# Kernel optimization log

Hardware: AMD Instinct MI355X
Metric: run time of the kernel (lower is better)

## Reference

```python
import math
import jax, jax.numpy as jnp
import numpy as np

B, N, M = 8, 2048, 1024
INPUT_SIZE = 512
HEAD_DIM = 64
NUM_HEADS = 6
ATTN_SIZE = HEAD_DIM * NUM_HEADS
MAX_CLASSES = 512


def setup_inputs() -> dict:
    key = jax.random.key(0)
    k1, k2, k3, k4, k5, k6, k7 = jax.random.split(key, 7)
    bound = 1.0 / math.sqrt(INPUT_SIZE)
    return {
        "train_embeddings": jax.random.normal(k1, (B, N, INPUT_SIZE), jnp.float32),
        "test_embeddings": jax.random.normal(k2, (B, M, INPUT_SIZE), jnp.float32),
        "targets": jax.random.randint(k3, (B, N), 0, MAX_CLASSES),
        # torch nn.Linear weights, stored as [in, out] for direct matmul
        "Wq": jax.random.uniform(k4, (INPUT_SIZE, ATTN_SIZE), jnp.float32, -bound, bound),
        "bq": jax.random.uniform(k5, (ATTN_SIZE,), jnp.float32, -bound, bound),
        "Wk": jax.random.uniform(k6, (INPUT_SIZE, ATTN_SIZE), jnp.float32, -bound, bound),
        "bk": jax.random.uniform(k7, (ATTN_SIZE,), jnp.float32, -bound, bound),
    }


def reference(train_embeddings, test_embeddings, targets, Wq, bq, Wk, bk):
    b, m, _ = test_embeddings.shape
    # projections -> [B, S, H, D]
    q_bmhd = (test_embeddings @ Wq + bq).reshape(b, m, NUM_HEADS, HEAD_DIM)
    k_bnhd = (train_embeddings @ Wk + bk).reshape(b, -1, NUM_HEADS, HEAD_DIM)
    scale = 1.0 / math.sqrt(HEAD_DIM)  # SDPA default scale
    # attention scores [B, H, M, N]
    scores = jnp.einsum("bmhd,bnhd->bhmn", q_bmhd, k_bnhd) * scale
    attn = jax.nn.softmax(scores, axis=-1)
    # one-hot train targets [B, N, C]; chunk-folding in the torch code is a
    # memory trick — mathematically it is just attn @ one_hot per head
    onehot_bnc = jax.nn.one_hot(targets, MAX_CLASSES, dtype=q_bmhd.dtype)
    out_bhmc = jnp.einsum("bhmn,bnc->bhmc", attn, onehot_bnc)
    out_bmc = out_bhmc.mean(axis=1)          # mean over heads
    out_mbc = out_bmc.transpose(1, 0, 2)      # [M, B, C]
    return jnp.log(jnp.clip(out_mbc, 1e-05) + 3e-05)
```

## Files before the change

kernel.cpp:

```cpp
#include <hip/hip_runtime.h>
#include <hip/hip_bf16.h>

#define BQ 8
#define NN 2048
#define MM 1024
#define EE 512
#define NH 6
#define AA 384
#define CC 512

#define KROW_B (AA * 2)
#define TILE_B (16 * KROW_B)
#define WROW_B (EE * 2)
#define WTILE_B (16 * WROW_B)

#define QSCALE 0.1803368801111204f

typedef __bf16 bf16x8 __attribute__((ext_vector_type(8)));
typedef float  f32x4  __attribute__((ext_vector_type(4)));
using bf16 = __hip_bfloat16;

static __device__ __forceinline__ f32x4 mfma16(bf16x8 a, bf16x8 b, f32x4 c) {
  return __builtin_amdgcn_mfma_f32_16x16x32_bf16(a, b, c, 0, 0, 0);
}

typedef __attribute__((address_space(1))) const void gconst_void;
typedef __attribute__((address_space(3))) void lds_void_t;
static __device__ __forceinline__ void ld_lds16(const void* g, void* l) {
  __builtin_amdgcn_global_load_lds((gconst_void*)g, (lds_void_t*)l, 16, 0, 0);
}

static __device__ __forceinline__ unsigned short f2bfu(float x) {
  union { __hip_bfloat16 h; unsigned short u; } v;
  v.h = __float2bfloat16(x);
  return v.u;
}
static __device__ __forceinline__ float bf2f(unsigned short u) {
  union { unsigned int i; float f; } x;
  x.i = ((unsigned int)u) << 16;
  return x.f;
}

__global__ __launch_bounds__(256) void transw_kernel(const float* __restrict__ W, bf16* __restrict__ WT) {
  __shared__ float t[64][65];
  int kb = (blockIdx.x / 6) * 64, nb = (blockIdx.x % 6) * 64;
  int tid = threadIdx.x;
  int lr = tid >> 4, lc = (tid & 15) * 4;
  #pragma unroll
  for (int p = 0; p < 4; p++) {
    int k = lr + p * 16;
    float4 v = *reinterpret_cast<const float4*>(W + (size_t)(kb + k) * AA + nb + lc);
    t[k][lc] = v.x; t[k][lc + 1] = v.y; t[k][lc + 2] = v.z; t[k][lc + 3] = v.w;
  }
  __syncthreads();
  #pragma unroll
  for (int p = 0; p < 4; p++) {
    int n = lr + p * 16;
    bf16* dst = WT + (size_t)(nb + n) * EE + kb + lc;
    dst[0] = __float2bfloat16(t[lc][n]);
    dst[1] = __float2bfloat16(t[lc + 1][n]);
    dst[2] = __float2bfloat16(t[lc + 2][n]);
    dst[3] = __float2bfloat16(t[lc + 3][n]);
  }
}

__global__ __launch_bounds__(512) void build_kernel(const int* __restrict__ targets,
                                                    int* __restrict__ offs, int* __restrict__ idxs) {
  __shared__ int cnt[CC], ssum[CC], pos[CC];
  int b = blockIdx.x, tid = threadIdx.x;
  cnt[tid] = 0;
  __syncthreads();
  int t[4];
  #pragma unroll
  for (int i = 0; i < 4; i++) {
    t[i] = targets[b * NN + tid * 4 + i];
    atomicAdd(&cnt[t[i]], 1);
  }
  __syncthreads();
  ssum[tid] = cnt[tid];
  __syncthreads();
  for (int d = 1; d < CC; d <<= 1) {
    int v = (tid >= d) ? ssum[tid - d] : 0;
    __syncthreads();
    ssum[tid] += v;
    __syncthreads();
  }
  int excl = ssum[tid] - cnt[tid];
  offs[b * (CC + 1) + tid] = excl;
  if (tid == CC - 1) offs[b * (CC + 1) + CC] = NN;
  pos[tid] = excl;
  __syncthreads();
  #pragma unroll
  for (int i = 0; i < 4; i++) {
    int p = atomicAdd(&pos[t[i]], 1);
    idxs[b * NN + p] = tid * 4 + i;
  }
}

__global__ __launch_bounds__(256, 3) void proj_kernel(
    const float* __restrict__ test, const float* __restrict__ train,
    const bf16* __restrict__ WqT, const bf16* __restrict__ WkT,
    const float* __restrict__ bq, const float* __restrict__ bk,
    bf16* __restrict__ Qb, bf16* __restrict__ Kb)
{
  __shared__ char wbuf[3][WTILE_B];
  int tid = threadIdx.x, wid = tid >> 6, lane = tid & 63;
  int bid = blockIdx.x;
  int sub = bid & 1, unit = bid >> 1;
  const float* A; const bf16* WT; const float* bias; bf16* C; float scale; int m0;
  if (unit < 128) { A = test;  WT = WqT; bias = bq; C = Qb; scale = QSCALE; m0 = unit * 64; }
  else            { A = train; WT = WkT; bias = bk; C = Kb; scale = 1.0f;   m0 = (unit - 128) * 64; }
  m0 += wid * 16;
  int row = lane & 15, hi = lane >> 4;

  bf16x8 af[16];
  const float* arow = A + (size_t)(m0 + row) * EE + hi * 8;
  #pragma unroll
  for (int ks = 0; ks < 16; ks++) {
    float4 u = *reinterpret_cast<const float4*>(arow + ks * 32);
    float4 v = *reinterpret_cast<const float4*>(arow + ks * 32 + 4);
    bf16x8 f;
    f[0] = (__bf16)u.x; f[1] = (__bf16)u.y; f[2] = (__bf16)u.z; f[3] = (__bf16)u.w;
    f[4] = (__bf16)v.x; f[5] = (__bf16)v.y; f[6] = (__bf16)v.z; f[7] = (__bf16)v.w;
    af[ks] = f;
  }

  int ldso[4], srco[4];
  #pragma unroll
  for (int i = 0; i < 4; i++) {
    int off = tid * 16 + i * 4096;
    int rw = off >> 10, c = off & 1023;
    ldso[i] = off;
    srco[i] = rw * WROW_B + (c ^ ((rw & 7) << 4));
  }
  const char* wgbase = (const char*)WT + (size_t)sub * 12 * WTILE_B;
  int sw = (row & 7) << 4;

  auto stage = [&](int t, int buf) {
    const char* src = wgbase + (size_t)t * WTILE_B;
    #pragma unroll
    for (int i = 0; i < 4; i++) ld_lds16(src + srco[i], wbuf[buf] + ldso[i]);
  };
  auto compute = [&](int buf, int t) {
    const char* wb = wbuf[buf] + row * WROW_B;
    f32x4 acc0 = {0.f, 0.f, 0.f, 0.f}, acc1 = {0.f, 0.f, 0.f, 0.f};
    #pragma unroll
    for (int ks = 0; ks < 16; ks += 2) {
      bf16x8 w0 = *reinterpret_cast<const bf16x8*>(wb + ((hi * 16 + ks * 64) ^ sw));
      bf16x8 w1 = *reinterpret_cast<const bf16x8*>(wb + ((hi * 16 + (ks + 1) * 64) ^ sw));
      acc0 = mfma16(af[ks], w0, acc0);
      acc1 = mfma16(af[ks + 1], w1, acc1);
    }
    f32x4 acc = acc0 + acc1;
    int ocol = (sub * 12 + t) * 16 + row;
    float bv = bias[ocol];
    #pragma unroll
    for (int j = 0; j < 4; j++)
      C[(size_t)(m0 + hi * 4 + j) * AA + ocol] = __float2bfloat16((acc[j] + bv) * scale);
  };

  stage(0, 0);
  stage(1, 1);
  asm volatile("s_waitcnt vmcnt(4)" ::: "memory");
  __builtin_amdgcn_s_barrier();
  __builtin_amdgcn_sched_barrier(0);
  stage(2, 2);
  compute(0, 0);

  int cur = 1, stg = 0;
  #pragma unroll 1
  for (int t = 1; t < 11; t++) {
    asm volatile("s_waitcnt vmcnt(8)" ::: "memory");
    __builtin_amdgcn_s_barrier();
    __builtin_amdgcn_sched_barrier(0);
    if (t < 10) stage(t + 2, stg);
    compute(cur, t);
    cur = cur + 1 < 3 ? cur + 1 : 0;
    stg = stg + 1 < 3 ? stg + 1 : 0;
  }
  asm volatile("s_waitcnt vmcnt(4)" ::: "memory");
  __builtin_amdgcn_s_barrier();
  __builtin_amdgcn_sched_barrier(0);
  compute(cur, 11);
}

__global__ __launch_bounds__(256, 4) void zpass_kernel(
    const bf16* __restrict__ Qb, const bf16* __restrict__ Kb, float* __restrict__ Zp)
{
  __shared__ char kbuf[3][TILE_B];
  int id = blockIdx.x;
  int b = id & 7, r = id >> 3, mt = r & 15, nc = r >> 4;
  int tid = threadIdx.x, wid = tid >> 6, lane = tid & 63;
  int m0 = mt * 64 + wid * 16, n0 = nc * 256;
  int row = lane & 15, hi = lane >> 4;

  bf16x8 qf[12];
  const bf16* qrow = Qb + ((size_t)(b * MM + m0 + row)) * AA + hi * 8;
  #pragma unroll
  for (int ks = 0; ks < 12; ks++) qf[ks] = *reinterpret_cast<const bf16x8*>(qrow + ks * 32);

  int ldso[3], srco[3];
  #pragma unroll
  for (int i = 0; i < 3; i++) {
    int off = wid * 3072 + i * 1024 + lane * 16;
    int rw = off / KROW_B, c = off - rw * KROW_B;
    ldso[i] = off;
    srco[i] = rw * KROW_B + (c ^ ((rw & 7) << 4));
  }
  const char* kgbase = (const char*)(Kb + ((size_t)(b * NN + n0)) * AA);

  int sw = (row & 7) << 4;
  int rbase = row * KROW_B;
  int x0 = rbase + ((hi * 16) ^ sw);
  int x1 = rbase + (((hi * 16) + 64) ^ sw);

  float zacc[NH][4];
  #pragma unroll
  for (int h = 0; h < NH; h++)
    #pragma unroll
    for (int j = 0; j < 4; j++) zacc[h][j] = 0.f;

  auto stage = [&](int t, int buf) {
    const char* src = kgbase + (size_t)t * TILE_B;
    #pragma unroll
    for (int i = 0; i < 3; i++) ld_lds16(src + srco[i], kbuf[buf] + ldso[i]);
  };
  auto compute = [&](int buf) {
    const char* kb = kbuf[buf];
    #pragma unroll
    for (int h = 0; h < NH; h++) {
      bf16x8 k0 = *reinterpret_cast<const bf16x8*>(kb + h * 128 + x0);
      bf16x8 k1 = *reinterpret_cast<const bf16x8*>(kb + h * 128 + x1);
      f32x4 acc = {0.f, 0.f, 0.f, 0.f};
      acc = mfma16(qf[2 * h], k0, acc);
      acc = mfma16(qf[2 * h + 1], k1, acc);
      #pragma unroll
      for (int j = 0; j < 4; j++) zacc[h][j] += __builtin_amdgcn_exp2f(acc[j]);
    }
  };

  stage(0, 0);
  stage(1, 1);
  int cur = 0, stg = 2;
  #pragma unroll 1
  for (int nt = 0; nt < 15; nt++) {
    asm volatile("s_waitcnt vmcnt(3)" ::: "memory");
    __builtin_amdgcn_s_barrier();
    __builtin_amdgcn_sched_barrier(0);
    if (nt < 14) stage(nt + 2, stg);
    compute(cur);
    cur = cur + 1 < 3 ? cur + 1 : 0;
    stg = stg + 1 < 3 ? stg + 1 : 0;
  }
  asm volatile("s_waitcnt vmcnt(0)" ::: "memory");
  __builtin_amdgcn_s_barrier();
  __builtin_amdgcn_sched_barrier(0);
  compute(cur);

  #pragma unroll
  for (int h = 0; h < NH; h++)
    #pragma unroll
    for (int j = 0; j < 4; j++) {
      float v = zacc[h][j];
      v += __shfl_xor(v, 1); v += __shfl_xor(v, 2);
      v += __shfl_xor(v, 4); v += __shfl_xor(v, 8);
      zacc[h][j] = v;
    }
  if (row == 0) {
    #pragma unroll
    for (int h = 0; h < NH; h++)
      #pragma unroll
      for (int j = 0; j < 4; j++)
        Zp[(((size_t)nc * 8 + b) * NH + h) * MM + m0 + hi * 4 + j] = zacc[h][j];
  }
}

__global__ __launch_bounds__(256, 4) void wpass_kernel(
    const bf16* __restrict__ Qb, const bf16* __restrict__ Kb,
    const float* __restrict__ Zp, bf16* __restrict__ W2)
{
  __shared__ char kbuf[3][TILE_B];
  int id = blockIdx.x;
  int b = id & 7, r = id >> 3, mt = r & 15, nc = r >> 4;
  int tid = threadIdx.x, wid = tid >> 6, lane = tid & 63;
  int m0 = mt * 64 + wid * 16, n0 = nc * 256;
  int row = lane & 15, hi = lane >> 4;

  bf16x8 qf[12];
  const bf16* qrow = Qb + ((size_t)(b * MM + m0 + row)) * AA + hi * 8;
  #pragma unroll
  for (int ks = 0; ks < 12; ks++) qf[ks] = *reinterpret_cast<const bf16x8*>(qrow + ks * 32);

  float rz[NH][4];
  #pragma unroll
  for (int h = 0; h < NH; h++) {
    f32x4 z = {0.f, 0.f, 0.f, 0.f};
    #pragma unroll
    for (int p = 0; p < 8; p++)
      z += *reinterpret_cast<const f32x4*>(Zp + (((size_t)p * 8 + b) * NH + h) * MM + m0 + hi * 4);
    #pragma unroll
    for (int j = 0; j < 4; j++) rz[h][j] = 1.0f / (6.0f * z[j]);
  }

  int ldso[3], srco[3];
  #pragma unroll
  for (int i = 0; i < 3; i++) {
    int off = wid * 3072 + i * 1024 + lane * 16;
    int rw = off / KROW_B, c = off - rw * KROW_B;
    ldso[i] = off;
    srco[i] = rw * KROW_B + (c ^ ((rw & 7) << 4));
  }
  const char* kgbase = (const char*)(Kb + ((size_t)(b * NN + n0)) * AA);

  int sw = (row & 7) << 4;
  int rbase = row * KROW_B;
  int x0 = rbase + ((hi * 16) ^ sw);
  int x1 = rbase + (((hi * 16) + 64) ^ sw);

  int m4 = (m0 >> 2) + hi;

  auto stage = [&](int t, int buf) {
    const char* src = kgbase + (size_t)t * TILE_B;
    #pragma unroll
    for (int i = 0; i < 3; i++) ld_lds16(src + srco[i], kbuf[buf] + ldso[i]);
  };
  auto compute = [&](int buf, int nt) {
    const char* kb = kbuf[buf];
    float w0 = 0.f, w1 = 0.f, w2 = 0.f, w3 = 0.f;
    #pragma unroll
    for (int h = 0; h < NH; h++) {
      bf16x8 k0 = *reinterpret_cast<const bf16x8*>(kb + h * 128 + x0);
      bf16x8 k1 = *reinterpret_cast<const bf16x8*>(kb + h * 128 + x1);
      f32x4 acc = {0.f, 0.f, 0.f, 0.f};
      acc = mfma16(qf[2 * h], k0, acc);
      acc = mfma16(qf[2 * h + 1], k1, acc);
      w0 += __builtin_amdgcn_exp2f(acc[0]) * rz[h][0];
      w1 += __builtin_amdgcn_exp2f(acc[1]) * rz[h][1];
      w2 += __builtin_amdgcn_exp2f(acc[2]) * rz[h][2];
      w3 += __builtin_amdgcn_exp2f(acc[3]) * rz[h][3];
    }
    int n = n0 + nt * 16 + row;
    ushort4 q;
    q.x = f2bfu(w0); q.y = f2bfu(w1); q.z = f2bfu(w2); q.w = f2bfu(w3);
    *reinterpret_cast<ushort4*>((unsigned short*)W2 + (((size_t)(b * 256 + m4)) * NN + n) * 4) = q;
  };

  stage(0, 0);
  stage(1, 1);
  asm volatile("s_waitcnt vmcnt(3)" ::: "memory");
  __builtin_amdgcn_s_barrier();
  __builtin_amdgcn_sched_barrier(0);
  stage(2, 2);
  compute(0, 0);

  int cur = 1, stg = 0;
  #pragma unroll 1
  for (int nt = 1; nt < 15; nt++) {
    asm volatile("s_waitcnt vmcnt(7)" ::: "memory");
    __builtin_amdgcn_s_barrier();
    __builtin_amdgcn_sched_barrier(0);
    if (nt < 14) stage(nt + 2, stg);
    compute(cur, nt);
    cur = cur + 1 < 3 ? cur + 1 : 0;
    stg = stg + 1 < 3 ? stg + 1 : 0;
  }
  asm volatile("s_waitcnt vmcnt(4)" ::: "memory");
  __builtin_amdgcn_s_barrier();
  __builtin_amdgcn_sched_barrier(0);
  compute(cur, 15);
}

__global__ __launch_bounds__(512) void gather_kernel(
    const bf16* __restrict__ W2, const int* __restrict__ offs,
    const int* __restrict__ idxs, float* __restrict__ out)
{
  __shared__ char wl[2 * NN * 8];
  __shared__ int ilb[NN];
  int id = blockIdx.x;
  int b = id & 7, mt = id >> 3;
  int g0 = mt * 2;
  int tid = threadIdx.x;

  const uint4* src = (const uint4*)((const unsigned short*)W2 + ((size_t)(b * 256 + g0)) * NN * 4);
  uint4* dst = (uint4*)wl;
  #pragma unroll
  for (int i = tid; i < 2 * NN * 8 / 16; i += 512) dst[i] = src[i];
  const int* il = idxs + b * NN;
  #pragma unroll
  for (int i = tid; i < NN; i += 512) ilb[i] = il[i];
  __syncthreads();

  int c = tid;
  int o0 = offs[b * (CC + 1) + c], o1 = offs[b * (CC + 1) + c + 1];
  #pragma unroll 1
  for (int g = 0; g < 2; g++) {
    float s0 = 0.f, s1 = 0.f, s2 = 0.f, s3 = 0.f;
    for (int i = o0; i < o1; i++) {
      int idx = ilb[i];
      ushort4 v = *reinterpret_cast<const ushort4*>(wl + g * (NN * 8) + idx * 8);
      s0 += bf2f(v.x); s1 += bf2f(v.y); s2 += bf2f(v.z); s3 += bf2f(v.w);
    }
    int m = mt * 8 + g * 4;
    out[((size_t)(m + 0) * BQ + b) * CC + c] = __logf(fmaxf(s0, 1e-5f) + 3e-5f);
    out[((size_t)(m + 1) * BQ + b) * CC + c] = __logf(fmaxf(s1, 1e-5f) + 3e-5f);
    out[((size_t)(m + 2) * BQ + b) * CC + c] = __logf(fmaxf(s2, 1e-5f) + 3e-5f);
    out[((size_t)(m + 3) * BQ + b) * CC + c] = __logf(fmaxf(s3, 1e-5f) + 3e-5f);
  }
}

extern "C" void kernel_launch(void* const* d_in, const int* in_sizes, int n_in,
                              void* d_out, int out_size, void* d_ws, size_t ws_size,
                              hipStream_t stream) {
  const float* train = (const float*)d_in[0];
  const float* test  = (const float*)d_in[1];
  const int*   tgt   = (const int*)d_in[2];
  const float* Wq    = (const float*)d_in[3];
  const float* bq    = (const float*)d_in[4];
  const float* Wk    = (const float*)d_in[5];
  const float* bk    = (const float*)d_in[6];
  float* out = (float*)d_out;

  char* ws = (char*)d_ws;
  bf16*  WqT  = (bf16*)(ws);
  bf16*  WkT  = (bf16*)(ws + 393216);
  bf16*  Qb   = (bf16*)(ws + 786432);
  bf16*  Kb   = (bf16*)(ws + 7077888);
  float* Zp   = (float*)(ws + 19660800);
  bf16*  Wbuf = (bf16*)(ws + 21233664);
  int*   offs = (int*)(ws + 54788096);
  int*   idxs = (int*)(ws + 54804512);

  transw_kernel<<<48, 256, 0, stream>>>(Wq, WqT);
  transw_kernel<<<48, 256, 0, stream>>>(Wk, WkT);
  build_kernel<<<BQ, 512, 0, stream>>>(tgt, offs, idxs);
  proj_kernel<<<768, 256, 0, stream>>>(test, train, WqT, WkT, bq, bk, Qb, Kb);
  zpass_kernel<<<1024, 256, 0, stream>>>(Qb, Kb, Zp);
  wpass_kernel<<<1024, 256, 0, stream>>>(Qb, Kb, Zp, Wbuf);
  gather_kernel<<<1024, 512, 0, stream>>>(Wbuf, offs, idxs, out);
}
```

Measured before the change: 112.8 us.

## Use double-buffered 32-row K stages with wave priority in z/w passes

The zpass and wpass kernels switch from a triple-buffered pipeline of 16-row K tiles to a double-buffered pipeline of 32-row tiles. This halves the number of barriers and waitcnt points per block. The compute sections are wrapped in s_setprio so MFMA/exp waves get issue priority, and occupancy hints drop from 4 to 3 blocks per CU to fit the larger LDS footprint. The trade-off is less prefetch depth, fewer resident waves, and a vmcnt(0) wait in zpass that exposes load latency.

New measurement: 112.3 us. Within noise of the previous version (-0.5%).

```diff
diff --git a/kernel.cpp b/kernel.cpp
--- a/kernel.cpp
+++ b/kernel.cpp
@@ -11,6 +11,7 @@
 
 #define KROW_B (AA * 2)
 #define TILE_B (16 * KROW_B)
+#define STILE_B (32 * KROW_B)
 #define WROW_B (EE * 2)
 #define WTILE_B (16 * WROW_B)
 
@@ -184,10 +185,10 @@
   compute(cur, 11);
 }
 
-__global__ __launch_bounds__(256, 4) void zpass_kernel(
+__global__ __launch_bounds__(256, 3) void zpass_kernel(
     const bf16* __restrict__ Qb, const bf16* __restrict__ Kb, float* __restrict__ Zp)
 {
-  __shared__ char kbuf[3][TILE_B];
+  __shared__ char kbuf[2][STILE_B];
   int id = blockIdx.x;
   int b = id & 7, r = id >> 3, mt = r & 15, nc = r >> 4;
   int tid = threadIdx.x, wid = tid >> 6, lane = tid & 63;
@@ -199,10 +200,10 @@
   #pragma unroll
   for (int ks = 0; ks < 12; ks++) qf[ks] = *reinterpret_cast<const bf16x8*>(qrow + ks * 32);
 
-  int ldso[3], srco[3];
-  #pragma unroll
-  for (int i = 0; i < 3; i++) {
-    int off = wid * 3072 + i * 1024 + lane * 16;
+  int ldso[6], srco[6];
+  #pragma unroll
+  for (int i = 0; i < 6; i++) {
+    int off = tid * 16 + i * 4096;
     int rw = off / KROW_B, c = off - rw * KROW_B;
     ldso[i] = off;
     srco[i] = rw * KROW_B + (c ^ ((rw & 7) << 4));
@@ -221,41 +222,44 @@
     for (int j = 0; j < 4; j++) zacc[h][j] = 0.f;
 
   auto stage = [&](int t, int buf) {
-    const char* src = kgbase + (size_t)t * TILE_B;
-    #pragma unroll
-    for (int i = 0; i < 3; i++) ld_lds16(src + srco[i], kbuf[buf] + ldso[i]);
+    const char* src = kgbase + (size_t)t * STILE_B;
+    #pragma unroll
+    for (int i = 0; i < 6; i++) ld_lds16(src + srco[i], kbuf[buf] + ldso[i]);
   };
   auto compute = [&](int buf) {
-    const char* kb = kbuf[buf];
-    #pragma unroll
-    for (int h = 0; h < NH; h++) {
-      bf16x8 k0 = *reinterpret_cast<const bf16x8*>(kb + h * 128 + x0);
-      bf16x8 k1 = *reinterpret_cast<const bf16x8*>(kb + h * 128 + x1);
-      f32x4 acc = {0.f, 0.f, 0.f, 0.f};
-      acc = mfma16(qf[2 * h], k0, acc);
-      acc = mfma16(qf[2 * h + 1], k1, acc);
+    __builtin_amdgcn_s_setprio(1);
+    #pragma unroll
+    for (int s = 0; s < 2; s++) {
+      const char* kb = kbuf[buf] + s * TILE_B;
       #pragma unroll
-      for (int j = 0; j < 4; j++) zacc[h][j] += __builtin_amdgcn_exp2f(acc[j]);
+      for (int h = 0; h < NH; h++) {
+        bf16x8 k0 = *reinterpret_cast<const bf16x8*>(kb + h * 128 + x0);
+        bf16x8 k1 = *reinterpret_cast<const bf16x8*>(kb + h * 128 + x1);
+        f32x4 acc = {0.f, 0.f, 0.f, 0.f};
+        acc = mfma16(qf[2 * h], k0, acc);
+        acc = mfma16(qf[2 * h + 1], k1, acc);
+        #pragma unroll
+        for (int j = 0; j < 4; j++) zacc[h][j] += __builtin_amdgcn_exp2f(acc[j]);
+      }
     }
+    __builtin_amdgcn_s_setprio(0);
   };
 
   stage(0, 0);
-  stage(1, 1);
-  int cur = 0, stg = 2;
-  #pragma unroll 1
-  for (int nt = 0; nt < 15; nt++) {
-    asm volatile("s_waitcnt vmcnt(3)" ::: "memory");
-    __builtin_amdgcn_s_barrier();
-    __builtin_amdgcn_sched_barrier(0);
-    if (nt < 14) stage(nt + 2, stg);
-    compute(cur);
-    cur = cur + 1 < 3 ? cur + 1 : 0;
-    stg = stg + 1 < 3 ? stg + 1 : 0;
-  }
   asm volatile("s_waitcnt vmcnt(0)" ::: "memory");
   __builtin_amdgcn_s_barrier();
   __builtin_amdgcn_sched_barrier(0);
-  compute(cur);
+  stage(1, 1);
+  compute(0);
+
+  #pragma unroll 1
+  for (int i = 1; i < 8; i++) {
+    asm volatile("s_waitcnt vmcnt(0)" ::: "memory");
+    __builtin_amdgcn_s_barrier();
+    __builtin_amdgcn_sched_barrier(0);
+    if (i < 7) stage(i + 1, (i + 1) & 1);
+    compute(i & 1);
+  }
 
   #pragma unroll
   for (int h = 0; h < NH; h++)
@@ -275,11 +279,11 @@
   }
 }
 
-__global__ __launch_bounds__(256, 4) void wpass_kernel(
+__global__ __launch_bounds__(256, 3) void wpass_kernel(
     const bf16* __restrict__ Qb, const bf16* __restrict__ Kb,
     const float* __restrict__ Zp, bf16* __restrict__ W2)
 {
-  __shared__ char kbuf[3][TILE_B];
+  __shared__ char kbuf[2][STILE_B];
   int id = blockIdx.x;
   int b = id & 7, r = id >> 3, mt = r & 15, nc = r >> 4;
   int tid = threadIdx.x, wid = tid >> 6, lane = tid & 63;
@@ -302,10 +306,10 @@
     for (int j = 0; j < 4; j++) rz[h][j] = 1.0f / (6.0f * z[j]);
   }
 
-  int ldso[3], srco[3];
-  #pragma unroll
-  for (int i = 0; i < 3; i++) {
-    int off = wid * 3072 + i * 1024 + lane * 16;
+  int ldso[6], srco[6];
+  #pragma unroll
+  for (int i = 0; i < 6; i++) {
+    int off = tid * 16 + i * 4096;
     int rw = off / KROW_B, c = off - rw * KROW_B;
     ldso[i] = off;
     srco[i] = rw * KROW_B + (c ^ ((rw & 7) << 4));
@@ -320,54 +324,51 @@
   int m4 = (m0 >> 2) + hi;
 
   auto stage = [&](int t, int buf) {
-    const char* src = kgbase + (size_t)t * TILE_B;
-    #pragma unroll
-    for (int i = 0; i < 3; i++) ld_lds16(src + srco[i], kbuf[buf] + ldso[i]);
-  };
-  auto compute = [&](int buf, int nt) {
-    const char* kb = kbuf[buf];
-    float w0 = 0.f, w1 = 0.f, w2 = 0.f, w3 = 0.f;
-    #pragma unroll
-    for (int h = 0; h < NH; h++) {
-      bf16x8 k0 = *reinterpret_cast<const bf16x8*>(kb + h * 128 + x0);
-      bf16x8 k1 = *reinterpret_cast<const bf16x8*>(kb + h * 128 + x1);
-      f32x4 acc = {0.f, 0.f, 0.f, 0.f};
-      acc = mfma16(qf[2 * h], k0, acc);
-      acc = mfma16(qf[2 * h + 1], k1, acc);
-      w0 += __builtin_amdgcn_exp2f(acc[0]) * rz[h][0];
-      w1 += __builtin_amdgcn_exp2f(acc[1]) * rz[h][1];
-      w2 += __builtin_amdgcn_exp2f(acc[2]) * rz[h][2];
-      w3 += __builtin_amdgcn_exp2f(acc[3]) * rz[h][3];
+    const char* src = kgbase + (size_t)t * STILE_B;
+    #pragma unroll
+    for (int i = 0; i < 6; i++) ld_lds16(src + srco[i], kbuf[buf] + ldso[i]);
+  };
+  auto compute = [&](int buf, int st) {
+    #pragma unroll
+    for (int s = 0; s < 2; s++) {
+      const char* kb = kbuf[buf] + s * TILE_B;
+      __builtin_amdgcn_s_setprio(1);
+      float w0 = 0.f, w1 = 0.f, w2 = 0.f, w3 = 0.f;
+      #pragma unroll
+      for (int h = 0; h < NH; h++) {
+        bf16x8 k0 = *reinterpret_cast<const bf16x8*>(kb + h * 128 + x0);
+        bf16x8 k1 = *reinterpret_cast<const bf16x8*>(kb + h * 128 + x1);
+        f32x4 acc = {0.f, 0.f, 0.f, 0.f};
+        acc = mfma16(qf[2 * h], k0, acc);
+        acc = mfma16(qf[2 * h + 1], k1, acc);
+        w0 += __builtin_amdgcn_exp2f(acc[0]) * rz[h][0];
+        w1 += __builtin_amdgcn_exp2f(acc[1]) * rz[h][1];
+        w2 += __builtin_amdgcn_exp2f(acc[2]) * rz[h][2];
+        w3 += __builtin_amdgcn_exp2f(acc[3]) * rz[h][3];
+      }
+      __builtin_amdgcn_s_setprio(0);
+      int n = n0 + (st * 2 + s) * 16 + row;
+      ushort4 q;
+      q.x = f2bfu(w0); q.y = f2bfu(w1); q.z = f2bfu(w2); q.w = f2bfu(w3);
+      *reinterpret_cast<ushort4*>((unsigned short*)W2 + (((size_t)(b * 256 + m4)) * NN + n) * 4) = q;
     }
-    int n = n0 + nt * 16 + row;
-    ushort4 q;
-    q.x = f2bfu(w0); q.y = f2bfu(w1); q.z = f2bfu(w2); q.w = f2bfu(w3);
-    *reinterpret_cast<ushort4*>((unsigned short*)W2 + (((size_t)(b * 256 + m4)) * NN + n) * 4) = q;
   };
 
   stage(0, 0);
-  stage(1, 1);
-  asm volatile("s_waitcnt vmcnt(3)" ::: "memory");
+  asm volatile("s_waitcnt vmcnt(0)" ::: "memory");
   __builtin_amdgcn_s_barrier();
   __builtin_amdgcn_sched_barrier(0);
-  stage(2, 2);
+  stage(1, 1);
   compute(0, 0);
 
-  int cur = 1, stg = 0;
   #pragma unroll 1
-  for (int nt = 1; nt < 15; nt++) {
-    asm volatile("s_waitcnt vmcnt(7)" ::: "memory");
+  for (int i = 1; i < 8; i++) {
+    asm volatile("s_waitcnt vmcnt(2)" ::: "memory");
     __builtin_amdgcn_s_barrier();
     __builtin_amdgcn_sched_barrier(0);
-    if (nt < 14) stage(nt + 2, stg);
-    compute(cur, nt);
-    cur = cur + 1 < 3 ? cur + 1 : 0;
-    stg = stg + 1 < 3 ? stg + 1 : 0;
-  }
-  asm volatile("s_waitcnt vmcnt(4)" ::: "memory");
-  __builtin_amdgcn_s_barrier();
-  __builtin_amdgcn_sched_barrier(0);
-  compute(cur, 15);
+    if (i < 7) stage(i + 1, (i + 1) & 1);
+    compute(i & 1, i);
+  }
 }
 
 __global__ __launch_bounds__(512) void gather_kernel(
```
